# Optimization experiments

Hardware: AMD Instinct MI355X
Metric: run time of the kernel (lower is better)

Reference implementation:

```python
import jax, jax.numpy as jnp
import numpy as np

H = 64  # hidden size per direction


def _lstm_dir(x, w_ih, w_hh, b_ih, b_hh, reverse):
    """Single-direction LSTM over x: [B, T, D] -> [B, T, H]. PyTorch gate order i,f,g,o."""
    B = x.shape[0]
    # Precompute input projections for all timesteps at once: [B, T, 4H]
    xg = jnp.einsum('btd,gd->btg', x, w_ih) + b_ih + b_hh

    def step(carry, xt):
        h, c = carry
        g = xt + h @ w_hh.T                       # [B, 4H]
        i, f, gc, o = jnp.split(g, 4, axis=-1)
        c = jax.nn.sigmoid(f) * c + jax.nn.sigmoid(i) * jnp.tanh(gc)
        h = jax.nn.sigmoid(o) * jnp.tanh(c)
        return (h, c), h

    init = (jnp.zeros((B, H), x.dtype), jnp.zeros((B, H), x.dtype))
    _, hs = jax.lax.scan(step, init, jnp.swapaxes(xg, 0, 1), reverse=reverse)
    return jnp.swapaxes(hs, 0, 1)  # [B, T, H]


def _bilstm(x, layer_params):
    out = x
    for (wif, whf, bif, bhf, wir, whr, bir, bhr) in layer_params:
        fwd = _lstm_dir(out, wif, whf, bif, bhf, reverse=False)
        bwd = _lstm_dir(out, wir, whr, bir, bhr, reverse=True)
        out = jnp.concatenate([fwd, bwd], axis=-1)  # [B, T, 2H]
    return out


def setup_inputs() -> dict:
    key = jax.random.key(0)
    ks = jax.random.split(key, 20)
    B, T, D = 1024, 256, 5
    s = 1.0 / np.sqrt(H)  # PyTorch LSTM init bound
    u = lambda k, shape: jax.random.uniform(k, shape, jnp.float32, -s, s)
    inp = {"x": jax.random.normal(ks[0], (B, T, D), jnp.float32)}
    dims = [D, 2 * H]
    i = 1
    for l in range(2):
        d = dims[l]
        for suf in ("", "r"):
            inp[f"w_ih_l{l}{suf}"] = u(ks[i], (4 * H, d)); i += 1
            inp[f"w_hh_l{l}{suf}"] = u(ks[i], (4 * H, H)); i += 1
            inp[f"b_ih_l{l}{suf}"] = u(ks[i], (4 * H,)); i += 1
            inp[f"b_hh_l{l}{suf}"] = u(ks[i], (4 * H,)); i += 1
    inp["fc_w"] = u(ks[17], (1, 2 * H))
    inp["fc_b"] = u(ks[18], (1,))
    return inp


def reference(x, w_ih_l0, w_hh_l0, b_ih_l0, b_hh_l0,
              w_ih_l0r, w_hh_l0r, b_ih_l0r, b_hh_l0r,
              w_ih_l1, w_hh_l1, b_ih_l1, b_hh_l1,
              w_ih_l1r, w_hh_l1r, b_ih_l1r, b_hh_l1r,
              fc_w, fc_b):
    layer_params = [
        (w_ih_l0, w_hh_l0, b_ih_l0, b_hh_l0, w_ih_l0r, w_hh_l0r, b_ih_l0r, b_hh_l0r),
        (w_ih_l1, w_hh_l1, b_ih_l1, b_hh_l1, w_ih_l1r, w_hh_l1r, b_ih_l1r, b_hh_l1r),
    ]
    out = _bilstm(x, layer_params)       # [B, T, 2H]
    last = out[:, -1, :]                 # [B, 2H]
    return last @ fc_w.T + fc_b          # [B, 1]
```

## Files before the change

kernel.cpp:

```cpp
#include <hip/hip_runtime.h>
#include <hip/hip_bf16.h>

#define HH 64
#define TT 256
#define NB 1024
#define GG 256
#define DD0 5
#define DD1 128

typedef __attribute__((ext_vector_type(8))) short bf16x8;
typedef __attribute__((ext_vector_type(4))) float f32x4;
typedef __attribute__((ext_vector_type(4))) unsigned int u32x4;

#define MFMA16(a, b, c) __builtin_amdgcn_mfma_f32_16x16x32_bf16((a), (b), (c), 0, 0, 0)

__device__ __forceinline__ void barrier_lds() {
    asm volatile("s_waitcnt lgkmcnt(0)\n\ts_barrier" ::: "memory");
}

__device__ __forceinline__ float rcp_fast(float x) {
    float r;
    asm("v_rcp_f32 %0, %1" : "=v"(r) : "v"(x));
    return r;
}
__device__ __forceinline__ float sigf(float x) { return rcp_fast(1.0f + __expf(-x)); }
__device__ __forceinline__ float tanh_fast(float x) { return 2.0f * rcp_fast(1.0f + __expf(-2.0f * x)) - 1.0f; }

__device__ __forceinline__ float bf2f(short s) {
    unsigned int u = ((unsigned int)(unsigned short)s) << 16;
    return __builtin_bit_cast(float, u);
}
__device__ __forceinline__ short f2bf_rne(float x) {
    unsigned int u = __builtin_bit_cast(unsigned int, x);
    u += 0x7fffu + ((u >> 16) & 1u);
    return (short)(u >> 16);
}

__device__ __forceinline__ int hsf_waddr(int u, int row) {
    return ((u >> 5) * 512) + (((u >> 3) & 3) * 128) + row * 8 + (u & 7);
}


__launch_bounds__(256, 1)
__global__ void lstm_l0(const float* __restrict__ x,
                        const float* __restrict__ w_ih_f, const float* __restrict__ w_hh_f,
                        const float* __restrict__ b_ih_f, const float* __restrict__ b_hh_f,
                        const float* __restrict__ w_ih_r, const float* __restrict__ w_hh_r,
                        const float* __restrict__ b_ih_r, const float* __restrict__ b_hh_r,
                        unsigned int* __restrict__ out0) {
    const int tid  = threadIdx.x;
    const int w    = tid >> 6;
    const int l    = tid & 63;
    const int col  = l & 15;
    const int rg   = l >> 4;
    const int dir  = blockIdx.x & 1;
    const int row0 = (blockIdx.x >> 1) * 8;
    const int u    = w * 16 + col;

    const float* w_ih = dir ? w_ih_r : w_ih_f;
    const float* w_hh = dir ? w_hh_r : w_hh_f;
    const float* b_ih = dir ? b_ih_r : b_ih_f;
    const float* b_hh = dir ? b_hh_r : b_hh_f;

    __shared__ __align__(16) unsigned int xsp[8 * 2056];
    __shared__ __align__(16) short hsf[2][2048];

    for (int i = tid; i < 8 * TT * DD0; i += 256) {
        const int row = i / (TT * DD0);
        const int rem = i - row * (TT * DD0);
        const int t = rem / DD0, d = rem - t * DD0;
        const float v = x[(size_t)row0 * TT * DD0 + i];
        const short hi = f2bf_rne(v);
        const short lo = f2bf_rne(v - bf2f(hi));
        xsp[row * 2056 + t * 8 + d] =
            (unsigned int)(unsigned short)hi | ((unsigned int)(unsigned short)lo << 16);
    }
    for (int i = tid; i < 2 * 2048; i += 256) ((short*)hsf)[i] = 0;

    bf16x8 whh_hi[4][2], whh_lo[4][2];
#pragma unroll
    for (int q = 0; q < 4; ++q) {
        const int gate = (w + 4 * q) * 16 + col;
#pragma unroll
        for (int ks = 0; ks < 2; ++ks) {
            const float* src = w_hh + gate * HH + ks * 32 + 8 * rg;
#pragma unroll
            for (int e = 0; e < 8; ++e) {
                float v = src[e];
                short h16 = f2bf_rne(v);
                whh_hi[q][ks][e] = h16;
                whh_lo[q][ks][e] = f2bf_rne(v - bf2f(h16));
            }
        }
    }
    bf16x8 wxb[4];
#pragma unroll
    for (int q = 0; q < 4; ++q) {
        const int gate = (w + 4 * q) * 16 + col;
        short whi[5], wlo[5];
#pragma unroll
        for (int d = 0; d < DD0; ++d) {
            float v = w_ih[gate * DD0 + d];
            whi[d] = f2bf_rne(v);
            wlo[d] = f2bf_rne(v - bf2f(whi[d]));
        }
        const float bbv = b_ih[gate] + b_hh[gate];
        const short bbh = f2bf_rne(bbv);
        const short bbl = f2bf_rne(bbv - bf2f(bbh));
        bf16x8 bs = {};
        if (rg == 0) {
            bs[0] = whi[0]; bs[1] = whi[1]; bs[2] = whi[2]; bs[3] = whi[3]; bs[4] = whi[4];
            bs[5] = whi[0]; bs[6] = whi[1]; bs[7] = whi[2];
        } else if (rg == 1) {
            bs[0] = whi[3]; bs[1] = whi[4];
            bs[2] = wlo[0]; bs[3] = wlo[1]; bs[4] = wlo[2]; bs[5] = wlo[3]; bs[6] = wlo[4];
            bs[7] = bbh;
        } else if (rg == 2) {
            bs[0] = bbl;
        }
        wxb[q] = bs;
    }

    bf16x8 xf = {};
    if (rg == 2) xf[0] = (short)0x3f80;

    unsigned int* po[4];
    const int t0 = dir ? (TT - 1) : 0;
#pragma unroll
    for (int r = 0; r < 4; ++r) {
        const int row = (rg & 1) * 4 + r;
        po[r] = out0 + ((size_t)(row0 + row) * TT + t0) * 128 + dir * 64 + u;
    }
    const int pstep = dir ? -128 : 128;

    f32x4 cc = {0.f, 0.f, 0.f, 0.f};
    __syncthreads();

    for (int t = 0; t < TT; ++t) {
        const int tt  = dir ? (TT - 1 - t) : t;
        const int cur = t & 1, nxt = cur ^ 1;

        if (rg < 2) {
            const unsigned int* pp = &xsp[(col & 7) * 2056 + tt * 8];
            const u32x4 p03 = *(const u32x4*)pp;
            const unsigned int p4 = pp[4];
            unsigned int w0, w1, w2, w3;
            if (rg == 0) {
                w0 = (p03[0] & 0xffffu) | (p03[1] << 16);
                w1 = (p03[2] & 0xffffu) | (p03[3] << 16);
                w2 = (p4 & 0xffffu)     | (p03[0] & 0xffff0000u);
                w3 = (p03[1] >> 16)     | (p03[2] & 0xffff0000u);
            } else {
                w0 = (p03[3] >> 16)     | (p4 & 0xffff0000u);
                w1 = (p03[0] & 0xffffu) | (p03[1] << 16);
                w2 = (p03[2] & 0xffffu) | (p03[3] << 16);
                w3 = (p4 & 0xffffu)     | 0x3f800000u;
            }
            u32x4 wv = {w0, w1, w2, w3};
            xf = __builtin_bit_cast(bf16x8, wv);
        }

        const short* hb = &hsf[cur][0];
        bf16x8 ah0 = *(const bf16x8*)&hb[0 * 512 + l * 8];
        bf16x8 ah1 = *(const bf16x8*)&hb[1 * 512 + l * 8];
        bf16x8 ah2 = *(const bf16x8*)&hb[2 * 512 + l * 8];
        bf16x8 ah3 = *(const bf16x8*)&hb[3 * 512 + l * 8];
        f32x4 acc[4];
#pragma unroll
        for (int q = 0; q < 4; ++q) {
            f32x4 a = {0.f, 0.f, 0.f, 0.f};
            a = MFMA16(xf, wxb[q], a);
            a = MFMA16(ah0, whh_hi[q][0], a);
            a = MFMA16(ah1, whh_hi[q][1], a);
            a = MFMA16(ah2, whh_hi[q][0], a);
            a = MFMA16(ah3, whh_hi[q][1], a);
            a = MFMA16(ah0, whh_lo[q][0], a);
            a = MFMA16(ah1, whh_lo[q][1], a);
            acc[q] = a;
        }
        if (rg < 2) {
#pragma unroll
            for (int r = 0; r < 4; ++r) {
                const int row = rg * 4 + r;
                const float cn = sigf(acc[1][r]) * cc[r] + sigf(acc[0][r]) * tanh_fast(acc[2][r]);
                const float hn = sigf(acc[3][r]) * tanh_fast(cn);
                cc[r] = cn;
                const short hi16 = f2bf_rne(hn);
                const short lo16 = f2bf_rne(hn - bf2f(hi16));
                const int wa = hsf_waddr(u, row);
                hsf[nxt][wa]        = hi16;
                hsf[nxt][wa + 1024] = lo16;
                *po[r] = (unsigned int)(unsigned short)hi16 |
                         ((unsigned int)(unsigned short)lo16 << 16);
                po[r] += pstep;
            }
        }
        barrier_lds();
    }
}

__launch_bounds__(512, 1)
__global__ void lstm_l1_pc(const unsigned int* __restrict__ h0,
                           const float* __restrict__ w_ih, const float* __restrict__ w_hh,
                           const float* __restrict__ b_ih, const float* __restrict__ b_hh,
                           float* __restrict__ h_last) {
    const int tid  = threadIdx.x;
    const int W    = tid >> 6;
    const int l    = tid & 63;
    const int col  = l & 15;
    const int rg   = l >> 4;
    const int row0 = blockIdx.x * 4;

    __shared__ __align__(16) short hsf2[2][4 * 144];
    __shared__ __align__(16) float ihaccf[2 * 4 * 64 * 20];
    __shared__ __align__(16) short wflo_s[4 * 4 * 4 * 512];

    for (int i = tid; i < 2 * 4 * 144; i += 512) ((short*)hsf2)[i] = 0;

    if (W < 4) {
        const int m = W;
        bf16x8 wf_hi[4][4];
        float bbq[4];
#pragma unroll
        for (int q = 0; q < 4; ++q) {
            const int gate = (m + 4 * q) * 16 + col;
            bbq[q] = b_ih[gate] + b_hh[gate];
#pragma unroll
            for (int ks = 0; ks < 4; ++ks) {
                const float* src = w_ih + gate * DD1 + ks * 32 + 8 * rg;
                bf16x8 hi, lo;
#pragma unroll
                for (int e = 0; e < 8; ++e) {
                    float v = src[e];
                    short h16 = f2bf_rne(v);
                    hi[e] = h16;
                    lo[e] = f2bf_rne(v - bf2f(h16));
                }
                wf_hi[q][ks] = hi;
                *(bf16x8*)&wflo_s[(((m * 4 + q) * 4 + ks) * 64 + l) * 8] = lo;
            }
        }
        const int arr = col & 3, aj = col >> 2;
        const unsigned int* xsrc = h0 + ((size_t)(row0 + arr) * TT + aj) * 128 + 8 * rg;

        bf16x8 xA[8], xB[8];
        auto loadx = [&](int tbase, bf16x8 (&xr)[8]) {
            const unsigned int* p = xsrc + (size_t)tbase * 128;
#pragma unroll
            for (int ks = 0; ks < 4; ++ks) {
                const u32x4 a0 = *(const u32x4*)&p[ks * 32];
                const u32x4 a1 = *(const u32x4*)&p[ks * 32 + 4];
                u32x4 hw = {(a0[0] & 0xffffu) | (a0[1] << 16), (a0[2] & 0xffffu) | (a0[3] << 16),
                            (a1[0] & 0xffffu) | (a1[1] << 16), (a1[2] & 0xffffu) | (a1[3] << 16)};
                u32x4 lw = {(a0[0] >> 16) | (a0[1] & 0xffff0000u), (a0[2] >> 16) | (a0[3] & 0xffff0000u),
                            (a1[0] >> 16) | (a1[1] & 0xffff0000u), (a1[2] >> 16) | (a1[3] & 0xffff0000u)};
                xr[ks]     = __builtin_bit_cast(bf16x8, hw);
                xr[4 + ks] = __builtin_bit_cast(bf16x8, lw);
            }
        };
        auto ih_q = [&](int q, const bf16x8 (&xr)[8], int buf) {
            bf16x8 wl0 = *(const bf16x8*)&wflo_s[(((m * 4 + q) * 4 + 0) * 64 + l) * 8];
            bf16x8 wl1 = *(const bf16x8*)&wflo_s[(((m * 4 + q) * 4 + 1) * 64 + l) * 8];
            bf16x8 wl2 = *(const bf16x8*)&wflo_s[(((m * 4 + q) * 4 + 2) * 64 + l) * 8];
            bf16x8 wl3 = *(const bf16x8*)&wflo_s[(((m * 4 + q) * 4 + 3) * 64 + l) * 8];
            f32x4 a0 = {0.f, 0.f, 0.f, 0.f};
            f32x4 a1 = {0.f, 0.f, 0.f, 0.f};
            f32x4 a2 = {0.f, 0.f, 0.f, 0.f};
#pragma unroll
            for (int ks = 0; ks < 4; ++ks) a0 = MFMA16(xr[ks],     wf_hi[q][ks], a0);
#pragma unroll
            for (int ks = 0; ks < 4; ++ks) a1 = MFMA16(xr[4 + ks], wf_hi[q][ks], a1);
            a2 = MFMA16(xr[0], wl0, a2);
            a2 = MFMA16(xr[1], wl1, a2);
            a2 = MFMA16(xr[2], wl2, a2);
            a2 = MFMA16(xr[3], wl3, a2);
            f32x4 a = (a0 + a1) + a2;
            a += bbq[q];
            const int ug = m * 16 + col;
            *(f32x4*)&ihaccf[((buf * 4 + rg) * 64 + ug) * 20 + q * 4] = a;
        };

        loadx(0, xA);
        ih_q(0, xA, 0); ih_q(1, xA, 0); ih_q(2, xA, 0); ih_q(3, xA, 0);
        loadx(4, xB);
        __syncthreads();

        for (int tb = 0; tb < TT; tb += 8) {
            if (tb + 8 < TT) loadx(tb + 8, xA);
            ih_q(0, xB, 1); barrier_lds();
            ih_q(1, xB, 1); barrier_lds();
            ih_q(2, xB, 1); barrier_lds();
            ih_q(3, xB, 1); barrier_lds();
            if (tb + 12 < TT) loadx(tb + 12, xB);
            const bool doih = (tb + 8 < TT);
            if (doih) ih_q(0, xA, 0);
            barrier_lds();
            if (doih) ih_q(1, xA, 0);
            barrier_lds();
            if (doih) ih_q(2, xA, 0);
            barrier_lds();
            if (doih) ih_q(3, xA, 0);
            barrier_lds();
        }
    } else {
        const int w = W - 4;
        const int u = w * 16 + col;
        const int g = rg;
        const int arow = (l & 15) >> 2;

        bf16x8 whh_hi[4][2], whh_lo[4][2];
#pragma unroll
        for (int q = 0; q < 4; ++q) {
            const int gate = (w + 4 * q) * 16 + col;
#pragma unroll
            for (int ks = 0; ks < 2; ++ks) {
                const float* src = w_hh + gate * HH + ks * 32 + 8 * rg;
#pragma unroll
                for (int e = 0; e < 8; ++e) {
                    float v = src[e];
                    short h16 = f2bf_rne(v);
                    whh_hi[q][ks][e] = h16;
                    whh_lo[q][ks][e] = f2bf_rne(v - bf2f(h16));
                }
            }
        }

        float cc = 0.f;
        __syncthreads();

        auto step = [&](int t, int k) {
            const int cur = k & 1, nxt = cur ^ 1;
            const int j = k & 3, ib = k >> 2;
            const float* ibase = &ihaccf[((ib * 4 + j) * 64 + u) * 20 + g];
            const float iv0 = ibase[0], iv1 = ibase[4], iv2 = ibase[8], iv3 = ibase[12];
            const short* hb = &hsf2[cur][0];
            bf16x8 ah0 = *(const bf16x8*)&hb[arow * 144 +  0 + 8 * rg];
            bf16x8 ah1 = *(const bf16x8*)&hb[arow * 144 + 32 + 8 * rg];
            bf16x8 ah2 = *(const bf16x8*)&hb[arow * 144 + 64 + 8 * rg];
            bf16x8 ah3 = *(const bf16x8*)&hb[arow * 144 + 96 + 8 * rg];
            f32x4 acc[4];
#pragma unroll
            for (int q = 0; q < 4; ++q) {
                f32x4 p0 = {0.f, 0.f, 0.f, 0.f};
                f32x4 p1 = {0.f, 0.f, 0.f, 0.f};
                p0 = MFMA16(ah0, whh_hi[q][0], p0);
                p1 = MFMA16(ah1, whh_hi[q][1], p1);
                p0 = MFMA16(ah2, whh_hi[q][0], p0);
                p1 = MFMA16(ah3, whh_hi[q][1], p1);
                p0 = MFMA16(ah0, whh_lo[q][0], p0);
                p1 = MFMA16(ah1, whh_lo[q][1], p1);
                acc[q] = p0 + p1;
            }
            const float gi_ = acc[0][0] + iv0;
            const float gf_ = acc[1][0] + iv1;
            const float gg_ = acc[2][0] + iv2;
            const float go_ = acc[3][0] + iv3;
            const float cn = sigf(gf_) * cc + sigf(gi_) * tanh_fast(gg_);
            const float hn = sigf(go_) * tanh_fast(cn);
            cc = cn;
            const short hi16 = f2bf_rne(hn);
            hsf2[nxt][g * 144 + u]      = hi16;
            hsf2[nxt][g * 144 + 64 + u] = f2bf_rne(hn - bf2f(hi16));
            if (t == TT - 1) h_last[(size_t)(row0 + g) * HH + u] = hn;
            barrier_lds();
        };

        for (int tb = 0; tb < TT; tb += 8) {
#pragma unroll
            for (int k = 0; k < 8; ++k) step(tb + k, k);
        }
    }
}

__global__ void lstm_tail(const unsigned int* __restrict__ in0,
                          const float* __restrict__ h1f,
                          const float* __restrict__ w_ih_r,
                          const float* __restrict__ b_ih_r, const float* __restrict__ b_hh_r,
                          const float* __restrict__ fc_w, const float* __restrict__ fc_b,
                          float* __restrict__ out) {
    const int b   = blockIdx.x;
    const int tid = threadIdx.x;
    __shared__ __align__(16) float insl[DD1];
    __shared__ __align__(16) float hb[HH];
    __shared__ __align__(16) float gsh[256];

    if (tid < DD1) {
        const unsigned int v = in0[((size_t)b * TT + (TT - 1)) * 128 + tid];
        insl[tid] = bf2f((short)(v & 0xffffu)) + bf2f((short)(v >> 16));
    }
    __syncthreads();

    float a0 = b_ih_r[tid] + b_hh_r[tid], a1 = 0.f, a2 = 0.f, a3 = 0.f;
    const float4* in4 = (const float4*)insl;
#pragma unroll
    for (int kk = 0; kk < 32; ++kk) {
        float4 iv = in4[kk];
        float4 wv = *(const float4*)&w_ih_r[tid * DD1 + 4 * kk];
        a0 += wv.x * iv.x;
        a1 += wv.y * iv.y;
        a2 += wv.z * iv.z;
        a3 += wv.w * iv.w;
    }
    gsh[tid] = (a0 + a1) + (a2 + a3);
    __syncthreads();

    if (tid < HH) {
        const float gi = gsh[tid], gc = gsh[tid + 128], go = gsh[tid + 192];
        const float ccv = sigf(gi) * tanh_fast(gc);
        hb[tid] = sigf(go) * tanh_fast(ccv);
    }
    __syncthreads();

    if (tid < 64) {
        float p = fc_w[tid] * h1f[(size_t)b * HH + tid] + fc_w[HH + tid] * hb[tid];
#pragma unroll
        for (int off = 32; off; off >>= 1) p += __shfl_xor(p, off);
        if (tid == 0) out[b] = p + fc_b[0];
    }
}

extern "C" void kernel_launch(void* const* d_in, const int* in_sizes, int n_in,
                              void* d_out, int out_size, void* d_ws, size_t ws_size,
                              hipStream_t stream) {
    const float* x = (const float*)d_in[0];
    char* ws = (char*)d_ws;
    const size_t out0_b = (size_t)NB * TT * 128 * 4;

    unsigned int* out0 = (unsigned int*)ws;
    float* h1f = (float*)(ws + out0_b);

    lstm_l0<<<256, 256, 0, stream>>>(
        x, (const float*)d_in[1], (const float*)d_in[2], (const float*)d_in[3], (const float*)d_in[4],
        (const float*)d_in[5], (const float*)d_in[6], (const float*)d_in[7], (const float*)d_in[8], out0);
    lstm_l1_pc<<<256, 512, 0, stream>>>(
        out0, (const float*)d_in[9], (const float*)d_in[10], (const float*)d_in[11],
        (const float*)d_in[12], h1f);
    lstm_tail<<<1024, 256, 0, stream>>>(
        out0, h1f, (const float*)d_in[13], (const float*)d_in[15], (const float*)d_in[16],
        (const float*)d_in[17], (const float*)d_in[18], (float*)d_out);
}
```

Baseline: 413.6 us.

## Restructure layer-0 LSTM: both directions per block, 4 rows, split MFMA chains

Layer 0 now runs both directions in one 512-thread block covering 4 batch rows, instead of one direction per 256-thread block covering 8 rows. The shared-memory h layout becomes padded per-row buffers. Each lane now handles one (row, unit) pair for the gate nonlinearities, so the per-step activation work is spread over all four row groups rather than two. The MFMA accumulation is split into two independent chains to shorten the dependency latency. The sequential critical path per step should get shorter, at the cost of more MFMA work spent on partially empty rows and a larger block.

Measured after the change: 389.3 us. 5.9% less time.

```diff
diff --git a/kernel.cpp b/kernel.cpp
--- a/kernel.cpp
+++ b/kernel.cpp
@@ -36,12 +36,8 @@
     return (short)(u >> 16);
 }
 
-__device__ __forceinline__ int hsf_waddr(int u, int row) {
-    return ((u >> 5) * 512) + (((u >> 3) & 3) * 128) + row * 8 + (u & 7);
-}
-
-
-__launch_bounds__(256, 1)
+
+__launch_bounds__(512, 1)
 __global__ void lstm_l0(const float* __restrict__ x,
                         const float* __restrict__ w_ih_f, const float* __restrict__ w_hh_f,
                         const float* __restrict__ b_ih_f, const float* __restrict__ b_hh_f,
@@ -49,12 +45,13 @@
                         const float* __restrict__ b_ih_r, const float* __restrict__ b_hh_r,
                         unsigned int* __restrict__ out0) {
     const int tid  = threadIdx.x;
-    const int w    = tid >> 6;
+    const int W    = tid >> 6;
+    const int dir  = W >> 2;
+    const int w    = W & 3;
     const int l    = tid & 63;
     const int col  = l & 15;
     const int rg   = l >> 4;
-    const int dir  = blockIdx.x & 1;
-    const int row0 = (blockIdx.x >> 1) * 8;
+    const int row0 = blockIdx.x * 4;
     const int u    = w * 16 + col;
 
     const float* w_ih = dir ? w_ih_r : w_ih_f;
@@ -62,10 +59,10 @@
     const float* b_ih = dir ? b_ih_r : b_ih_f;
     const float* b_hh = dir ? b_hh_r : b_hh_f;
 
-    __shared__ __align__(16) unsigned int xsp[8 * 2056];
-    __shared__ __align__(16) short hsf[2][2048];
-
-    for (int i = tid; i < 8 * TT * DD0; i += 256) {
+    __shared__ __align__(16) unsigned int xsp[4 * 2056];
+    __shared__ __align__(16) short hsf2[2][2][4 * 144];
+
+    for (int i = tid; i < 4 * TT * DD0; i += 512) {
         const int row = i / (TT * DD0);
         const int rem = i - row * (TT * DD0);
         const int t = rem / DD0, d = rem - t * DD0;
@@ -75,7 +72,7 @@
         xsp[row * 2056 + t * 8 + d] =
             (unsigned int)(unsigned short)hi | ((unsigned int)(unsigned short)lo << 16);
     }
-    for (int i = tid; i < 2 * 2048; i += 256) ((short*)hsf)[i] = 0;
+    for (int i = tid; i < 2 * 2 * 4 * 144; i += 512) ((short*)hsf2)[i] = 0;
 
     bf16x8 whh_hi[4][2], whh_lo[4][2];
 #pragma unroll
@@ -124,16 +121,12 @@
     bf16x8 xf = {};
     if (rg == 2) xf[0] = (short)0x3f80;
 
-    unsigned int* po[4];
     const int t0 = dir ? (TT - 1) : 0;
-#pragma unroll
-    for (int r = 0; r < 4; ++r) {
-        const int row = (rg & 1) * 4 + r;
-        po[r] = out0 + ((size_t)(row0 + row) * TT + t0) * 128 + dir * 64 + u;
-    }
+    unsigned int* po = out0 + ((size_t)(row0 + rg) * TT + t0) * 128 + dir * 64 + u;
     const int pstep = dir ? -128 : 128;
 
-    f32x4 cc = {0.f, 0.f, 0.f, 0.f};
+    const int arow = col >> 2;
+    float cc = 0.f;
     __syncthreads();
 
     for (int t = 0; t < TT; ++t) {
@@ -141,7 +134,7 @@
         const int cur = t & 1, nxt = cur ^ 1;
 
         if (rg < 2) {
-            const unsigned int* pp = &xsp[(col & 7) * 2056 + tt * 8];
+            const unsigned int* pp = &xsp[arow * 2056 + tt * 8];
             const u32x4 p03 = *(const u32x4*)pp;
             const unsigned int p4 = pp[4];
             unsigned int w0, w1, w2, w3;
@@ -160,41 +153,35 @@
             xf = __builtin_bit_cast(bf16x8, wv);
         }
 
-        const short* hb = &hsf[cur][0];
-        bf16x8 ah0 = *(const bf16x8*)&hb[0 * 512 + l * 8];
-        bf16x8 ah1 = *(const bf16x8*)&hb[1 * 512 + l * 8];
-        bf16x8 ah2 = *(const bf16x8*)&hb[2 * 512 + l * 8];
-        bf16x8 ah3 = *(const bf16x8*)&hb[3 * 512 + l * 8];
+        const short* hb = &hsf2[dir][cur][0];
+        bf16x8 ah0 = *(const bf16x8*)&hb[arow * 144 +  0 + 8 * rg];
+        bf16x8 ah1 = *(const bf16x8*)&hb[arow * 144 + 32 + 8 * rg];
+        bf16x8 ah2 = *(const bf16x8*)&hb[arow * 144 + 64 + 8 * rg];
+        bf16x8 ah3 = *(const bf16x8*)&hb[arow * 144 + 96 + 8 * rg];
         f32x4 acc[4];
 #pragma unroll
         for (int q = 0; q < 4; ++q) {
-            f32x4 a = {0.f, 0.f, 0.f, 0.f};
-            a = MFMA16(xf, wxb[q], a);
-            a = MFMA16(ah0, whh_hi[q][0], a);
-            a = MFMA16(ah1, whh_hi[q][1], a);
-            a = MFMA16(ah2, whh_hi[q][0], a);
-            a = MFMA16(ah3, whh_hi[q][1], a);
-            a = MFMA16(ah0, whh_lo[q][0], a);
-            a = MFMA16(ah1, whh_lo[q][1], a);
-            acc[q] = a;
-        }
-        if (rg < 2) {
-#pragma unroll
-            for (int r = 0; r < 4; ++r) {
-                const int row = rg * 4 + r;
-                const float cn = sigf(acc[1][r]) * cc[r] + sigf(acc[0][r]) * tanh_fast(acc[2][r]);
-                const float hn = sigf(acc[3][r]) * tanh_fast(cn);
-                cc[r] = cn;
-                const short hi16 = f2bf_rne(hn);
-                const short lo16 = f2bf_rne(hn - bf2f(hi16));
-                const int wa = hsf_waddr(u, row);
-                hsf[nxt][wa]        = hi16;
-                hsf[nxt][wa + 1024] = lo16;
-                *po[r] = (unsigned int)(unsigned short)hi16 |
-                         ((unsigned int)(unsigned short)lo16 << 16);
-                po[r] += pstep;
-            }
-        }
+            f32x4 p0 = {0.f, 0.f, 0.f, 0.f};
+            f32x4 p1 = {0.f, 0.f, 0.f, 0.f};
+            p0 = MFMA16(xf, wxb[q], p0);
+            p1 = MFMA16(ah0, whh_hi[q][0], p1);
+            p0 = MFMA16(ah1, whh_hi[q][1], p0);
+            p1 = MFMA16(ah2, whh_hi[q][0], p1);
+            p0 = MFMA16(ah3, whh_hi[q][1], p0);
+            p1 = MFMA16(ah0, whh_lo[q][0], p1);
+            p0 = MFMA16(ah1, whh_lo[q][1], p0);
+            acc[q] = p0 + p1;
+        }
+        const float cn = sigf(acc[1][0]) * cc + sigf(acc[0][0]) * tanh_fast(acc[2][0]);
+        const float hn = sigf(acc[3][0]) * tanh_fast(cn);
+        cc = cn;
+        const short hi16 = f2bf_rne(hn);
+        const short lo16 = f2bf_rne(hn - bf2f(hi16));
+        hsf2[dir][nxt][rg * 144 + u]      = hi16;
+        hsf2[dir][nxt][rg * 144 + 64 + u] = lo16;
+        *po = (unsigned int)(unsigned short)hi16 |
+              ((unsigned int)(unsigned short)lo16 << 16);
+        po += pstep;
         barrier_lds();
     }
 }
@@ -429,7 +416,7 @@
     unsigned int* out0 = (unsigned int*)ws;
     float* h1f = (float*)(ws + out0_b);
 
-    lstm_l0<<<256, 256, 0, stream>>>(
+    lstm_l0<<<256, 512, 0, stream>>>(
         x, (const float*)d_in[1], (const float*)d_in[2], (const float*)d_in[3], (const float*)d_in[4],
         (const float*)d_in[5], (const float*)d_in[6], (const float*)d_in[7], (const float*)d_in[8], out0);
     lstm_l1_pc<<<256, 512, 0, stream>>>(
```
